# Kernel optimization log

Measured on AMD Instinct MI355X. Metric: run time of the kernel, lower is better.

The kernel has to match this reference:

```python
import jax, jax.numpy as jnp
import numpy as np

N_NODES = 100000
N_EDGES = 1200000
IN_CH = 64


def setup_inputs() -> dict:
    key = jax.random.key(0)
    ks = jax.random.split(key, 6)
    scale = 1.0 / np.sqrt(IN_CH)
    return {
        "x": jax.random.normal(ks[0], (N_NODES, IN_CH), dtype=jnp.float32),
        "edge_index": jax.random.randint(ks[1], (2, N_EDGES), 0, N_NODES, dtype=jnp.int64),
        "W_gcn": jax.random.normal(ks[2], (IN_CH, IN_CH), dtype=jnp.float32) * scale,
        "b_gcn": jnp.zeros((IN_CH,), dtype=jnp.float32),
        "W1": jax.random.normal(ks[3], (IN_CH, 32), dtype=jnp.float32) * scale,
        "b1": jnp.zeros((32,), dtype=jnp.float32),
        "W2": jax.random.normal(ks[4], (32, 32), dtype=jnp.float32) * (1.0 / np.sqrt(32)),
        "b2": jnp.zeros((32,), dtype=jnp.float32),
        "W3": jax.random.normal(ks[5], (32, 2), dtype=jnp.float32) * (1.0 / np.sqrt(32)),
        "b3": jnp.zeros((2,), dtype=jnp.float32),
    }


def _gcn_conv(x, edge_index, W, b):
    # PyG GCNConv: add self-loops, symmetric normalization D^-1/2 A D^-1/2 (X W) + b
    N = x.shape[0]
    loop = jnp.arange(N, dtype=edge_index.dtype)
    src = jnp.concatenate([edge_index[0], loop])
    dst = jnp.concatenate([edge_index[1], loop])
    deg = jax.ops.segment_sum(jnp.ones_like(dst, dtype=x.dtype), dst, num_segments=N)
    d_inv_sqrt = jax.lax.rsqrt(deg)  # deg >= 1 thanks to self-loops
    norm = d_inv_sqrt[src] * d_inv_sqrt[dst]  # [E+N]
    h = x @ W  # [N, C]
    msg = h[src] * norm[:, None]  # gather + scale, [E+N, C]
    agg = jax.ops.segment_sum(msg, dst, num_segments=N)  # scatter-add, [N, C]
    return agg + b


def reference(x, edge_index, W_gcn, b_gcn, W1, b1, W2, b2, W3, b3):
    out = jax.nn.relu(_gcn_conv(x, edge_index, W_gcn, b_gcn))
    h = out + x  # residual
    h = jax.nn.relu(h @ W1 + b1)
    h = jax.nn.relu(h @ W2 + b2)
    return h @ W3 + b3  # [N, 2]
```

## Files before the change

kernel.cpp:

```cpp
#include <hip/hip_runtime.h>

#define NN 100000
#define CH 64
#define CAP 64
#define NPART 8
#define PSIZE ((NN + NPART - 1) / NPART)
#define FILLB 640

__global__ __launch_bounds__(256) void k_fill(const int* __restrict__ src,
                                              const int* __restrict__ dst,
                                              unsigned* __restrict__ cnt,
                                              int* __restrict__ bsrc, int E) {
    int part = blockIdx.x & (NPART - 1);
    int blk  = blockIdx.x >> 3;
    int lo = part * PSIZE, hi = lo + PSIZE;
    for (int e = blk * 256 + threadIdx.x; e < E; e += FILLB * 256) {
        int d = __builtin_nontemporal_load(dst + e);
        if (d >= lo && d < hi) {
            int s = __builtin_nontemporal_load(src + e);
            unsigned pos = atomicAdd(&cnt[d], 1u);
            if (pos < CAP) bsrc[(size_t)d * CAP + pos] = s;
        }
    }
}

__global__ void k_dinv(const unsigned* __restrict__ cnt, float* __restrict__ dinv, int N) {
    int i = blockIdx.x * blockDim.x + threadIdx.x;
    if (i < N) dinv[i] = rsqrtf((float)cnt[i] + 1.0f);
}

__global__ __launch_bounds__(256) void k_at(
        const unsigned* __restrict__ cnt, const int* __restrict__ bsrc,
        const float* __restrict__ dinv, const float* __restrict__ x,
        const float* __restrict__ Wg, const float* __restrict__ bgcn,
        const float* __restrict__ W1, const float* __restrict__ b1,
        const float* __restrict__ W2, const float* __restrict__ b2,
        const float* __restrict__ W3, const float* __restrict__ b3,
        float* __restrict__ out, int N) {
    __shared__ float R1[4096];
    __shared__ float R2[64 * 65];
    __shared__ float R3[64 * 33];
    __shared__ float bgs[64];
    int t = threadIdx.x;
    int nbase = blockIdx.x * 64;

    for (int i = t; i < 4096; i += 256) R1[i] = Wg[i];
    if (t < 64) bgs[t] = bgcn[t];

    {
        int nl = t >> 2, q = t & 3;
        int n = nbase + nl;
        float* r2p = R2 + nl * 65 + q * 16;
        if (n < N) {
            int c = (int)cnt[n]; if (c > CAP) c = CAP;
            const int* bp = bsrc + (size_t)n * CAP;
            float dn = dinv[n];
            float acc[16];
#pragma unroll
            for (int j = 0; j < 16; ++j) acc[j] = 0.f;
#pragma unroll 2
            for (int e = 0; e < c; ++e) {
                int s = bp[e];
                float w = dinv[s];
                const float4* xp = (const float4*)(x + (size_t)s * CH) + q * 4;
                float4 v0 = xp[0], v1 = xp[1], v2 = xp[2], v3 = xp[3];
                acc[0]  += v0.x * w; acc[1]  += v0.y * w; acc[2]  += v0.z * w; acc[3]  += v0.w * w;
                acc[4]  += v1.x * w; acc[5]  += v1.y * w; acc[6]  += v1.z * w; acc[7]  += v1.w * w;
                acc[8]  += v2.x * w; acc[9]  += v2.y * w; acc[10] += v2.z * w; acc[11] += v2.w * w;
                acc[12] += v3.x * w; acc[13] += v3.y * w; acc[14] += v3.z * w; acc[15] += v3.w * w;
            }
            const float4* xq = (const float4*)(x + (size_t)n * CH) + q * 4;
            float4 u0 = xq[0], u1 = xq[1], u2 = xq[2], u3 = xq[3];
            r2p[0]  = dn * (acc[0]  + u0.x * dn); r2p[1]  = dn * (acc[1]  + u0.y * dn);
            r2p[2]  = dn * (acc[2]  + u0.z * dn); r2p[3]  = dn * (acc[3]  + u0.w * dn);
            r2p[4]  = dn * (acc[4]  + u1.x * dn); r2p[5]  = dn * (acc[5]  + u1.y * dn);
            r2p[6]  = dn * (acc[6]  + u1.z * dn); r2p[7]  = dn * (acc[7]  + u1.w * dn);
            r2p[8]  = dn * (acc[8]  + u2.x * dn); r2p[9]  = dn * (acc[9]  + u2.y * dn);
            r2p[10] = dn * (acc[10] + u2.z * dn); r2p[11] = dn * (acc[11] + u2.w * dn);
            r2p[12] = dn * (acc[12] + u3.x * dn); r2p[13] = dn * (acc[13] + u3.y * dn);
            r2p[14] = dn * (acc[14] + u3.z * dn); r2p[15] = dn * (acc[15] + u3.w * dn);
        } else {
#pragma unroll
            for (int j = 0; j < 16; ++j) r2p[j] = 0.f;
        }
    }
    __syncthreads();

    int cg = t & 15, ng = t >> 4;
    float accv[4][4];
#pragma unroll
    for (int i = 0; i < 4; ++i)
#pragma unroll
        for (int u = 0; u < 4; ++u) accv[i][u] = 0.f;
    for (int k = 0; k < 64; ++k) {
        float wv0 = R1[k * 64 + cg * 4 + 0];
        float wv1 = R1[k * 64 + cg * 4 + 1];
        float wv2 = R1[k * 64 + cg * 4 + 2];
        float wv3 = R1[k * 64 + cg * 4 + 3];
        float va = R2[(ng * 4 + 0) * 65 + k];
        float vb = R2[(ng * 4 + 1) * 65 + k];
        float vc = R2[(ng * 4 + 2) * 65 + k];
        float vd = R2[(ng * 4 + 3) * 65 + k];
        accv[0][0] += va * wv0; accv[0][1] += va * wv1; accv[0][2] += va * wv2; accv[0][3] += va * wv3;
        accv[1][0] += vb * wv0; accv[1][1] += vb * wv1; accv[1][2] += vb * wv2; accv[1][3] += vb * wv3;
        accv[2][0] += vc * wv0; accv[2][1] += vc * wv1; accv[2][2] += vc * wv2; accv[2][3] += vc * wv3;
        accv[3][0] += vd * wv0; accv[3][1] += vd * wv1; accv[3][2] += vd * wv2; accv[3][3] += vd * wv3;
    }
    __syncthreads();

    for (int i = t; i < 2048; i += 256) R1[i] = W1[i];
    for (int i = t; i < 1024; i += 256) R1[2048 + i] = W2[i];
    if (t < 64) R1[3072 + t] = W3[t];
    if (t < 32) { R1[3136 + t] = b1[t]; R1[3168 + t] = b2[t]; }
    if (t < 2) R1[3200 + t] = b3[t];
#pragma unroll
    for (int i = 0; i < 4; ++i) {
        int nl2 = ng * 4 + i;
        int gr = nbase + nl2;
        float4 xv = make_float4(0.f, 0.f, 0.f, 0.f);
        if (gr < N) xv = *((const float4*)(x + (size_t)gr * CH) + cg);
        float* rp = R2 + nl2 * 65 + cg * 4;
        rp[0] = fmaxf(accv[i][0] + bgs[cg * 4 + 0], 0.f) + xv.x;
        rp[1] = fmaxf(accv[i][1] + bgs[cg * 4 + 1], 0.f) + xv.y;
        rp[2] = fmaxf(accv[i][2] + bgs[cg * 4 + 2], 0.f) + xv.z;
        rp[3] = fmaxf(accv[i][3] + bgs[cg * 4 + 3], 0.f) + xv.w;
    }
    __syncthreads();

    int nl = t & 63, g = t >> 6;
    {
        float a[8];
#pragma unroll
        for (int j = 0; j < 8; ++j) a[j] = R1[3136 + 8 * g + j];
        for (int k = 0; k < 64; ++k) {
            float v = R2[nl * 65 + k];
#pragma unroll
            for (int j = 0; j < 8; ++j)
                a[j] += v * R1[k * 32 + 8 * g + j];
        }
#pragma unroll
        for (int j = 0; j < 8; ++j) R3[nl * 33 + 8 * g + j] = a[j];
    }
    __syncthreads();

    {
        float a[8];
#pragma unroll
        for (int j = 0; j < 8; ++j) a[j] = R1[3168 + 8 * g + j];
        for (int k = 0; k < 32; ++k) {
            float v = fmaxf(R3[nl * 33 + k], 0.0f);
#pragma unroll
            for (int j = 0; j < 8; ++j)
                a[j] += v * R1[2048 + k * 32 + 8 * g + j];
        }
#pragma unroll
        for (int j = 0; j < 8; ++j) R2[nl * 65 + 8 * g + j] = a[j];
    }
    __syncthreads();

    if (t < 128) {
        int nl4 = t >> 1, g4 = t & 1;
        int gr = nbase + nl4;
        if (gr < N) {
            float y = R1[3200 + g4];
#pragma unroll
            for (int k = 0; k < 32; ++k)
                y += fmaxf(R2[nl4 * 65 + k], 0.0f) * R1[3072 + k * 2 + g4];
            out[(size_t)gr * 2 + g4] = y;
        }
    }
}

extern "C" void kernel_launch(void* const* d_in, const int* in_sizes, int n_in,
                              void* d_out, int out_size, void* d_ws, size_t ws_size,
                              hipStream_t stream) {
    const float* x  = (const float*)d_in[0];
    const int*   ei = (const int*)d_in[1];
    const float* Wg = (const float*)d_in[2];
    const float* bg = (const float*)d_in[3];
    const float* W1 = (const float*)d_in[4];
    const float* b1 = (const float*)d_in[5];
    const float* W2 = (const float*)d_in[6];
    const float* b2 = (const float*)d_in[7];
    const float* W3 = (const float*)d_in[8];
    const float* b3 = (const float*)d_in[9];
    float* out = (float*)d_out;

    const int N = NN;
    const int E = in_sizes[1] / 2;
    const int* src = ei;
    const int* dst = ei + E;

    char* base = (char*)d_ws;
    size_t o = 0;
    auto alloc = [&](size_t bytes) { void* p = base + o; o = (o + bytes + 255) & ~(size_t)255; return p; };
    unsigned* cnt  = (unsigned*)alloc((size_t)N * 4);
    float*    dinv = (float*)alloc((size_t)N * 4);
    int*      bsrc = (int*)alloc((size_t)N * CAP * 4);

    hipMemsetAsync(cnt, 0, (size_t)N * 4, stream);

    k_fill<<<NPART * FILLB, 256, 0, stream>>>(src, dst, cnt, bsrc, E);
    k_dinv<<<(N + 255) / 256, 256, 0, stream>>>(cnt, dinv, N);
    k_at<<<(N + 63) / 64, 256, 0, stream>>>(cnt, bsrc, dinv, x, Wg, bg,
                                            W1, b1, W2, b2, W3, b3, out, N);
}
```

Before: 235.4 us.

## Gather neighbor features in bf16 and vectorize edge-index loads in fill

A prep kernel converts x to bf16 and also computes dinv, so the neighbor gather in the aggregation reads half the bytes per edge. The self term still uses fp32 x. k_fill now loads src and dst four at a time as int4, with a tail loop for leftover edges, and no longer uses nontemporal loads. Precision of the aggregated messages drops to bf16 inputs, which adds a risk to accuracy, and the conversion pass costs extra traffic of its own.

```diff
diff --git a/kernel.cpp b/kernel.cpp
--- a/kernel.cpp
+++ b/kernel.cpp
@@ -6,6 +6,15 @@
 #define NPART 8
 #define PSIZE ((NN + NPART - 1) / NPART)
 #define FILLB 640
+
+__device__ __forceinline__ float bf_lo(unsigned u) { return __uint_as_float(u << 16); }
+__device__ __forceinline__ float bf_hi(unsigned u) { return __uint_as_float(u & 0xffff0000u); }
+
+__device__ __forceinline__ unsigned short f2bf(float f) {
+    unsigned u = __float_as_uint(f);
+    u += 0x7fffu + ((u >> 16) & 1u);
+    return (unsigned short)(u >> 16);
+}
 
 __global__ __launch_bounds__(256) void k_fill(const int* __restrict__ src,
                                               const int* __restrict__ dst,
@@ -14,24 +23,46 @@
     int part = blockIdx.x & (NPART - 1);
     int blk  = blockIdx.x >> 3;
     int lo = part * PSIZE, hi = lo + PSIZE;
-    for (int e = blk * 256 + threadIdx.x; e < E; e += FILLB * 256) {
-        int d = __builtin_nontemporal_load(dst + e);
-        if (d >= lo && d < hi) {
-            int s = __builtin_nontemporal_load(src + e);
-            unsigned pos = atomicAdd(&cnt[d], 1u);
-            if (pos < CAP) bsrc[(size_t)d * CAP + pos] = s;
-        }
-    }
-}
-
-__global__ void k_dinv(const unsigned* __restrict__ cnt, float* __restrict__ dinv, int N) {
+    int E4 = E >> 2;
+    const int4* src4 = (const int4*)src;
+    const int4* dst4 = (const int4*)dst;
+    for (int i = blk * 256 + threadIdx.x; i < E4; i += FILLB * 256) {
+        int4 d4 = dst4[i];
+        int4 s4 = src4[i];
+        if (d4.x >= lo && d4.x < hi) { unsigned p = atomicAdd(&cnt[d4.x], 1u); if (p < CAP) bsrc[(size_t)d4.x * CAP + p] = s4.x; }
+        if (d4.y >= lo && d4.y < hi) { unsigned p = atomicAdd(&cnt[d4.y], 1u); if (p < CAP) bsrc[(size_t)d4.y * CAP + p] = s4.y; }
+        if (d4.z >= lo && d4.z < hi) { unsigned p = atomicAdd(&cnt[d4.z], 1u); if (p < CAP) bsrc[(size_t)d4.z * CAP + p] = s4.z; }
+        if (d4.w >= lo && d4.w < hi) { unsigned p = atomicAdd(&cnt[d4.w], 1u); if (p < CAP) bsrc[(size_t)d4.w * CAP + p] = s4.w; }
+    }
+    if (part == 0 && blk == 0) {
+        for (int e = E4 * 4 + threadIdx.x; e < E; e += 256) {
+            int d = dst[e];
+            int s = src[e];
+            unsigned p = atomicAdd(&cnt[d], 1u);
+            if (p < CAP) bsrc[(size_t)d * CAP + p] = s;
+        }
+    }
+}
+
+__global__ __launch_bounds__(256) void k_prep(const float* __restrict__ x,
+                                              unsigned short* __restrict__ xb,
+                                              const unsigned* __restrict__ cnt,
+                                              float* __restrict__ dinv, int N) {
     int i = blockIdx.x * blockDim.x + threadIdx.x;
+    int tot4 = N * CH / 4;
+    if (i < tot4) {
+        float4 v = ((const float4*)x)[i];
+        ushort4 o;
+        o.x = f2bf(v.x); o.y = f2bf(v.y); o.z = f2bf(v.z); o.w = f2bf(v.w);
+        ((ushort4*)xb)[i] = o;
+    }
     if (i < N) dinv[i] = rsqrtf((float)cnt[i] + 1.0f);
 }
 
 __global__ __launch_bounds__(256) void k_at(
         const unsigned* __restrict__ cnt, const int* __restrict__ bsrc,
         const float* __restrict__ dinv, const float* __restrict__ x,
+        const unsigned short* __restrict__ xb,
         const float* __restrict__ Wg, const float* __restrict__ bgcn,
         const float* __restrict__ W1, const float* __restrict__ b1,
         const float* __restrict__ W2, const float* __restrict__ b2,
@@ -62,12 +93,16 @@
             for (int e = 0; e < c; ++e) {
                 int s = bp[e];
                 float w = dinv[s];
-                const float4* xp = (const float4*)(x + (size_t)s * CH) + q * 4;
-                float4 v0 = xp[0], v1 = xp[1], v2 = xp[2], v3 = xp[3];
-                acc[0]  += v0.x * w; acc[1]  += v0.y * w; acc[2]  += v0.z * w; acc[3]  += v0.w * w;
-                acc[4]  += v1.x * w; acc[5]  += v1.y * w; acc[6]  += v1.z * w; acc[7]  += v1.w * w;
-                acc[8]  += v2.x * w; acc[9]  += v2.y * w; acc[10] += v2.z * w; acc[11] += v2.w * w;
-                acc[12] += v3.x * w; acc[13] += v3.y * w; acc[14] += v3.z * w; acc[15] += v3.w * w;
+                const uint4* xp = (const uint4*)(xb + (size_t)s * CH) + q * 2;
+                uint4 A = xp[0], B = xp[1];
+                acc[0]  += bf_lo(A.x) * w; acc[1]  += bf_hi(A.x) * w;
+                acc[2]  += bf_lo(A.y) * w; acc[3]  += bf_hi(A.y) * w;
+                acc[4]  += bf_lo(A.z) * w; acc[5]  += bf_hi(A.z) * w;
+                acc[6]  += bf_lo(A.w) * w; acc[7]  += bf_hi(A.w) * w;
+                acc[8]  += bf_lo(B.x) * w; acc[9]  += bf_hi(B.x) * w;
+                acc[10] += bf_lo(B.y) * w; acc[11] += bf_hi(B.y) * w;
+                acc[12] += bf_lo(B.z) * w; acc[13] += bf_hi(B.z) * w;
+                acc[14] += bf_lo(B.w) * w; acc[15] += bf_hi(B.w) * w;
             }
             const float4* xq = (const float4*)(x + (size_t)n * CH) + q * 4;
             float4 u0 = xq[0], u1 = xq[1], u2 = xq[2], u3 = xq[3];
@@ -194,14 +229,16 @@
     char* base = (char*)d_ws;
     size_t o = 0;
     auto alloc = [&](size_t bytes) { void* p = base + o; o = (o + bytes + 255) & ~(size_t)255; return p; };
-    unsigned* cnt  = (unsigned*)alloc((size_t)N * 4);
-    float*    dinv = (float*)alloc((size_t)N * 4);
-    int*      bsrc = (int*)alloc((size_t)N * CAP * 4);
+    unsigned*       cnt  = (unsigned*)alloc((size_t)N * 4);
+    float*          dinv = (float*)alloc((size_t)N * 4);
+    int*            bsrc = (int*)alloc((size_t)N * CAP * 4);
+    unsigned short* xb   = (unsigned short*)alloc((size_t)N * CH * 2);
 
     hipMemsetAsync(cnt, 0, (size_t)N * 4, stream);
 
     k_fill<<<NPART * FILLB, 256, 0, stream>>>(src, dst, cnt, bsrc, E);
-    k_dinv<<<(N + 255) / 256, 256, 0, stream>>>(cnt, dinv, N);
-    k_at<<<(N + 63) / 64, 256, 0, stream>>>(cnt, bsrc, dinv, x, Wg, bg,
+    int prep_blocks = (N * CH / 4 + 255) / 256;
+    k_prep<<<prep_blocks, 256, 0, stream>>>(x, xb, cnt, dinv, N);
+    k_at<<<(N + 63) / 64, 256, 0, stream>>>(cnt, bsrc, dinv, x, xb, Wg, bg,
                                             W1, b1, W2, b2, W3, b3, out, N);
 }
```

Result: faster. 218.5 us (-7.2%).
